# Performance work log

Measured on AMD Instinct MI355X. Metric: run time of the kernel, lower is better.

Reference implementation:

```python
import jax, jax.numpy as jnp
import numpy as np

# Conv2d config matching init_kwargs
STRIDE = (1, 1)
PADDING = (1, 1)
DILATION = (1, 1)


def setup_inputs() -> dict:
    key = jax.random.key(0)
    k1, k2, k3 = jax.random.split(key, 3)
    B, Cin, H, W_ = 32, 128, 56, 56
    Cout, KH, KW = 256, 3, 3
    x = jax.random.normal(k1, (B, Cin, H, W_), dtype=jnp.float32)
    # original init: uniform(-stdv, stdv), stdv = 1/sqrt(Cin*KH*KW)
    stdv = 1.0 / np.sqrt(Cin * KH * KW)
    W = jax.random.uniform(k2, (Cout, Cin, KH, KW), dtype=jnp.float32, minval=-stdv, maxval=stdv)
    b = jax.random.uniform(k3, (Cout,), dtype=jnp.float32, minval=-stdv, maxval=stdv)
    return {"x": x, "W": W, "b": b}


def reference(x, W, b):
    # Same math as unfold(im2col) + GEMM + bias: a standard 2D convolution.
    out = jax.lax.conv_general_dilated(
        x, W,
        window_strides=STRIDE,
        padding=[(PADDING[0], PADDING[0]), (PADDING[1], PADDING[1])],
        rhs_dilation=DILATION,
        dimension_numbers=("NCHW", "OIHW", "NCHW"),
    )
    return out + b[None, :, None, None]
```

## Files before the change

kernel.cpp:

```cpp
#include <hip/hip_runtime.h>

typedef unsigned short ushort_t;
typedef __attribute__((ext_vector_type(8))) short bf16x8;
typedef __attribute__((ext_vector_type(4))) float f32x4;
typedef __attribute__((ext_vector_type(4))) unsigned short ushort4v;

constexpr int BATCH = 32, CIN = 128, H = 56, W = 56, COUT = 256;
constexpr int HP = 58, WP = 58;
constexpr int KTOT = CIN * 9;
constexpr size_t WB_BYTES = (size_t)COUT * KTOT * 2;
constexpr int PLANE = BATCH * HP * WP;
constexpr size_t XP_BYTES = (size_t)16 * PLANE * 8 * 2;

__device__ inline ushort_t f2bf(float f) {
  union { float fl; unsigned u; } v; v.fl = f;
  unsigned u = v.u;
  return (ushort_t)((u + 0x7fffu + ((u >> 16) & 1u)) >> 16);
}


__global__ void conv_w(const float* __restrict__ Ws, ushort_t* __restrict__ Wb2) {
  int idx = blockIdx.x * 256 + threadIdx.x;
  int c = idx & 7;
  int cout = (idx >> 3) & 255;
  int kb = (idx >> 11) & 7;
  int t = idx >> 14;
  int pos = t >> 1, half = t & 1;
  int cin = half * 64 + kb * 8 + c;
  Wb2[idx] = f2bf(Ws[(cout * 128 + cin) * 9 + pos]);
}

__global__ void xpad2(const float* __restrict__ x, ushort_t* __restrict__ xp2) {
  __shared__ ushort_t tile[128][58];
  int bh = blockIdx.x;
  int b = bh / 58, h = bh - b * 58;
  bool interior = (h >= 1 && h <= 56);
  if (interior) {
    int hIn = h - 1;
    const float4* x4 = (const float4*)x;
    {
      int ch = threadIdx.x & 127, side = threadIdx.x >> 7;
      tile[ch][side * 57] = 0;
    }
    for (int it = 0; it < 7; ++it) {
      int i = it * 256 + (int)threadIdx.x;
      int ch = i / 14, q = i - ch * 14;
      float4 v = x4[(size_t)(b * 128 + ch) * 784 + hIn * 14 + q];
      int wb = 1 + q * 4;
      tile[ch][wb + 0] = f2bf(v.x);
      tile[ch][wb + 1] = f2bf(v.y);
      tile[ch][wb + 2] = f2bf(v.z);
      tile[ch][wb + 3] = f2bf(v.w);
    }
  }
  __syncthreads();
  ushort4v* o4 = (ushort4v*)xp2;
  for (int it = 0; it < 8; ++it) {
    int i = it * 256 + (int)threadIdx.x;
    if (i >= 1856) break;
    int c8 = i / 116, r = i - c8 * 116;
    int w = r >> 1, hf = r & 1;
    ushort4v v;
    if (interior) {
      int ch = c8 * 8 + hf * 4;
      v.x = tile[ch + 0][w];
      v.y = tile[ch + 1][w];
      v.z = tile[ch + 2][w];
      v.w = tile[ch + 3][w];
    } else {
      v.x = v.y = v.z = v.w = 0;
    }
    o4[((size_t)((c8 * 32 + b) * 58 + h) * 58 + w) * 2 + hf] = v;
  }
}


__global__ __launch_bounds__(256, 2) void conv_mfma(
    const ushort_t* __restrict__ Wb2, const ushort_t* __restrict__ xp2,
    const float* __restrict__ bias, float* __restrict__ out) {
  __shared__ ushort_t ldsA[2][8192];
  __shared__ ushort_t ldsB[2][8192];

  const int tid = threadIdx.x;
  const int lane = tid & 63;
  const int wid = tid >> 6;
  const int wm = wid >> 1, wn = wid & 1;
  const int lg = lane >> 4, lr = lane & 15;
  const int tileN = blockIdx.x;
  const int blkM = blockIdx.y;

  const int srow = tid & 127;
  const int hi = tid >> 7;

  const ushort_t* aPre[4];
  const ushort_t* bPre[4];
  {
    int pg = tileN * 128 + srow;
    int bq = pg / 3136;
    int rem = pg - bq * 3136;
    int hh = rem / 56;
    int wwp = rem - hh * 56;
    int pixBase = (bq * 58 + hh) * 58 + wwp;
#pragma unroll
    for (int p = 0; p < 4; ++p) {
      int kb = p * 2 + hi;
      aPre[p] = Wb2 + kb * 2048 + blkM * 1024 + srow * 8;
      bPre[p] = xp2 + ((size_t)kb * PLANE + pixBase) * 8;
    }
  }
  const int dOff = tid * 8;

  f32x4 acc[4][4] = {};

  auto stage = [&](int bb, int t) {
    int pos = t >> 1;
    int kh = pos / 3;
    int kw = pos - kh * 3;
    int aoff = t * 16384;
    int xoff = ((t & 1) * (8 * PLANE) + kh * 58 + kw) * 8;
    ushort_t* dA = &ldsA[bb][0];
    ushort_t* dB = &ldsB[bb][0];
#pragma unroll
    for (int p = 0; p < 4; ++p) {
      __builtin_amdgcn_global_load_lds(
          (const __attribute__((address_space(1))) unsigned int*)(aPre[p] + aoff),
          (__attribute__((address_space(3))) unsigned int*)(dA + p * 2048 + dOff),
          16, 0, 0);
      __builtin_amdgcn_global_load_lds(
          (const __attribute__((address_space(1))) unsigned int*)(bPre[p] + xoff),
          (__attribute__((address_space(3))) unsigned int*)(dB + p * 2048 + dOff),
          16, 0, 0);
    }
  };

  auto compute = [&](int bb) {
    const ushort_t* A0 = &ldsA[bb][0];
    const ushort_t* B0 = &ldsB[bb][0];
#pragma unroll
    for (int ks = 0; ks < 2; ++ks) {
      const int kb = ks * 4 + lg;
      bf16x8 av[4], bv[4];
#pragma unroll
      for (int m = 0; m < 4; ++m)
        av[m] = *(const bf16x8*)(A0 + kb * 1024 + (wm * 64 + m * 16 + lr) * 8);
#pragma unroll
      for (int n = 0; n < 4; ++n)
        bv[n] = *(const bf16x8*)(B0 + kb * 1024 + (wn * 64 + n * 16 + lr) * 8);
#pragma unroll
      for (int m = 0; m < 4; ++m)
#pragma unroll
        for (int n = 0; n < 4; ++n)
          acc[m][n] = __builtin_amdgcn_mfma_f32_16x16x32_bf16(av[m], bv[n], acc[m][n], 0, 0, 0);
    }
  };

  stage(0, 0);
  int bb = 0;
  for (int t = 0; t < 18; ++t) {
    __syncthreads();
    if (t < 17) stage(bb ^ 1, t + 1);
    compute(bb);
    bb ^= 1;
  }

  const int cb = blkM * 128 + wm * 64 + lg * 4;
  float bvv[4][4];
#pragma unroll
  for (int m = 0; m < 4; ++m)
#pragma unroll
    for (int r = 0; r < 4; ++r) bvv[m][r] = bias[cb + m * 16 + r];

#pragma unroll
  for (int n = 0; n < 4; ++n) {
    int pgo = tileN * 128 + wn * 64 + n * 16 + lr;
    int bq2 = pgo / 3136;
    int rem2 = pgo - bq2 * 3136;
    float* op = out + (size_t)bq2 * 256 * 3136 + rem2;
#pragma unroll
    for (int m = 0; m < 4; ++m)
#pragma unroll
      for (int r = 0; r < 4; ++r)
        op[(size_t)(cb + m * 16 + r) * 3136] = acc[m][n][r] + bvv[m][r];
  }
}

__global__ void conv_naive(const float* __restrict__ x, const float* __restrict__ Wt,
                           const float* __restrict__ bias, float* __restrict__ out, int total) {
  int idx = blockIdx.x * 256 + threadIdx.x;
  if (idx >= total) return;
  int w = idx % 56;
  int t1 = idx / 56;
  int h = t1 % 56;
  int t2 = t1 / 56;
  int co = t2 % 256;
  int b = t2 / 256;
  float acc = bias[co];
  for (int c = 0; c < 128; ++c)
    for (int kh = 0; kh < 3; ++kh) {
      int ih = h + kh - 1;
      if (ih < 0 || ih >= 56) continue;
      for (int kw = 0; kw < 3; ++kw) {
        int iw = w + kw - 1;
        if (iw < 0 || iw >= 56) continue;
        acc += x[((b * 128 + c) * 56 + ih) * 56 + iw] * Wt[((co * 128 + c) * 3 + kh) * 3 + kw];
      }
    }
  out[idx] = acc;
}

extern "C" void kernel_launch(void* const* d_in, const int* in_sizes, int n_in,
                              void* d_out, int out_size, void* d_ws, size_t ws_size,
                              hipStream_t stream) {
  const float* x = (const float*)d_in[0];
  const float* Wt = (const float*)d_in[1];
  const float* bias = (const float*)d_in[2];
  float* out = (float*)d_out;

  const size_t need = WB_BYTES + XP_BYTES;
  if (ws_size < need) {
    int total = BATCH * COUT * H * W;
    conv_naive<<<(total + 255) / 256, 256, 0, stream>>>(x, Wt, bias, out, total);
    return;
  }
  ushort_t* Wb2 = (ushort_t*)d_ws;
  ushort_t* xp2 = (ushort_t*)((char*)d_ws + WB_BYTES);

  conv_w<<<1152, 256, 0, stream>>>(Wt, Wb2);
  xpad2<<<32 * 58, 256, 0, stream>>>(x, xp2);
  dim3 grid(784, 2);
  conv_mfma<<<grid, 256, 0, stream>>>(Wb2, xp2, bias, out);
}
```

Baseline: 230.7 us.

## Enlarge conv GEMM tile to 256x256 with 512 threads and prefetch two stages ahead

The implicit-GEMM conv kernel now uses 512-thread blocks, each covering all 256 output channels and 256 pixels. This replaces the 128x128 tiles spread over a 784x2 grid. Each wave computes an 8x4 grid of MFMA tiles, which raises compute per LDS read and means each pixel tile is loaded once instead of twice. The loop is restructured so global-to-LDS loads for step t+2 are issued after a barrier, overlapping with the second k-half of MFMAs, with explicit vmcnt waits and raised wave priority during the MFMA burst. The risks are 128 accumulator registers per thread, lower occupancy with 128KB of LDS per block, and only 392 blocks to fill the GPU.

```diff
diff --git a/kernel.cpp b/kernel.cpp
--- a/kernel.cpp
+++ b/kernel.cpp
@@ -75,109 +75,133 @@
 }
 
 
-__global__ __launch_bounds__(256, 2) void conv_mfma(
+__global__ __launch_bounds__(512) void conv_mfma(
     const ushort_t* __restrict__ Wb2, const ushort_t* __restrict__ xp2,
     const float* __restrict__ bias, float* __restrict__ out) {
-  __shared__ ushort_t ldsA[2][8192];
-  __shared__ ushort_t ldsB[2][8192];
+  __shared__ ushort_t ldsA[2][16384];
+  __shared__ ushort_t ldsB[2][16384];
 
   const int tid = threadIdx.x;
   const int lane = tid & 63;
   const int wid = tid >> 6;
-  const int wm = wid >> 1, wn = wid & 1;
+  const int wm = wid >> 2, wn = wid & 3;
   const int lg = lane >> 4, lr = lane & 15;
   const int tileN = blockIdx.x;
-  const int blkM = blockIdx.y;
-
-  const int srow = tid & 127;
-  const int hi = tid >> 7;
-
-  const ushort_t* aPre[4];
-  const ushort_t* bPre[4];
-  {
-    int pg = tileN * 128 + srow;
+
+  const ushort_t* aSrc[4];
+  const ushort_t* bSrc[4];
+#pragma unroll
+  for (int p = 0; p < 4; ++p) {
+    int idx = p * 512 + tid;
+    aSrc[p] = Wb2 + idx * 8;
+    int kb = idx >> 8, pi = idx & 255;
+    int pg = tileN * 256 + pi;
     int bq = pg / 3136;
     int rem = pg - bq * 3136;
     int hh = rem / 56;
-    int wwp = rem - hh * 56;
-    int pixBase = (bq * 58 + hh) * 58 + wwp;
-#pragma unroll
-    for (int p = 0; p < 4; ++p) {
-      int kb = p * 2 + hi;
-      aPre[p] = Wb2 + kb * 2048 + blkM * 1024 + srow * 8;
-      bPre[p] = xp2 + ((size_t)kb * PLANE + pixBase) * 8;
-    }
+    int ww = rem - hh * 56;
+    int pixBase = (bq * 58 + hh) * 58 + ww;
+    bSrc[p] = xp2 + ((size_t)kb * PLANE + pixBase) * 8;
   }
   const int dOff = tid * 8;
-
-  f32x4 acc[4][4] = {};
 
   auto stage = [&](int bb, int t) {
     int pos = t >> 1;
     int kh = pos / 3;
     int kw = pos - kh * 3;
     int aoff = t * 16384;
-    int xoff = ((t & 1) * (8 * PLANE) + kh * 58 + kw) * 8;
+    int boff = (t & 1) * (8 * PLANE * 8) + (kh * 58 + kw) * 8;
     ushort_t* dA = &ldsA[bb][0];
     ushort_t* dB = &ldsB[bb][0];
 #pragma unroll
     for (int p = 0; p < 4; ++p) {
       __builtin_amdgcn_global_load_lds(
-          (const __attribute__((address_space(1))) unsigned int*)(aPre[p] + aoff),
-          (__attribute__((address_space(3))) unsigned int*)(dA + p * 2048 + dOff),
+          (const __attribute__((address_space(1))) unsigned int*)(aSrc[p] + aoff),
+          (__attribute__((address_space(3))) unsigned int*)(dA + p * 4096 + dOff),
           16, 0, 0);
       __builtin_amdgcn_global_load_lds(
-          (const __attribute__((address_space(1))) unsigned int*)(bPre[p] + xoff),
-          (__attribute__((address_space(3))) unsigned int*)(dB + p * 2048 + dOff),
+          (const __attribute__((address_space(1))) unsigned int*)(bSrc[p] + boff),
+          (__attribute__((address_space(3))) unsigned int*)(dB + p * 4096 + dOff),
           16, 0, 0);
     }
   };
 
-  auto compute = [&](int bb) {
-    const ushort_t* A0 = &ldsA[bb][0];
-    const ushort_t* B0 = &ldsB[bb][0];
-#pragma unroll
-    for (int ks = 0; ks < 2; ++ks) {
-      const int kb = ks * 4 + lg;
-      bf16x8 av[4], bv[4];
-#pragma unroll
-      for (int m = 0; m < 4; ++m)
-        av[m] = *(const bf16x8*)(A0 + kb * 1024 + (wm * 64 + m * 16 + lr) * 8);
-#pragma unroll
-      for (int n = 0; n < 4; ++n)
-        bv[n] = *(const bf16x8*)(B0 + kb * 1024 + (wn * 64 + n * 16 + lr) * 8);
-#pragma unroll
-      for (int m = 0; m < 4; ++m)
-#pragma unroll
-        for (int n = 0; n < 4; ++n)
-          acc[m][n] = __builtin_amdgcn_mfma_f32_16x16x32_bf16(av[m], bv[n], acc[m][n], 0, 0, 0);
-    }
-  };
+  f32x4 acc[8][4] = {};
 
   stage(0, 0);
-  int bb = 0;
+  stage(1, 1);
+  asm volatile("s_waitcnt vmcnt(8)" ::: "memory");
+  __builtin_amdgcn_s_barrier();
+
   for (int t = 0; t < 18; ++t) {
-    __syncthreads();
-    if (t < 17) stage(bb ^ 1, t + 1);
-    compute(bb);
-    bb ^= 1;
-  }
-
-  const int cb = blkM * 128 + wm * 64 + lg * 4;
-  float bvv[4][4];
-#pragma unroll
-  for (int m = 0; m < 4; ++m)
+    const int p = t & 1;
+    const ushort_t* A0 = &ldsA[p][0];
+    const ushort_t* B0 = &ldsB[p][0];
+
+    bf16x8 a0[8], b0[4];
+    {
+      const int kb = lg;
+#pragma unroll
+      for (int m = 0; m < 8; ++m)
+        a0[m] = *(const bf16x8*)(A0 + kb * 2048 + (wm * 128 + m * 16 + lr) * 8);
+#pragma unroll
+      for (int n = 0; n < 4; ++n)
+        b0[n] = *(const bf16x8*)(B0 + kb * 2048 + (wn * 64 + n * 16 + lr) * 8);
+    }
+#pragma unroll
+    for (int m = 0; m < 8; ++m)
+#pragma unroll
+      for (int n = 0; n < 4; ++n)
+        acc[m][n] = __builtin_amdgcn_mfma_f32_16x16x32_bf16(a0[m], b0[n], acc[m][n], 0, 0, 0);
+
+    bf16x8 a1[8], b1[4];
+    {
+      const int kb = 4 + lg;
+#pragma unroll
+      for (int m = 0; m < 8; ++m)
+        a1[m] = *(const bf16x8*)(A0 + kb * 2048 + (wm * 128 + m * 16 + lr) * 8);
+#pragma unroll
+      for (int n = 0; n < 4; ++n)
+        b1[n] = *(const bf16x8*)(B0 + kb * 2048 + (wn * 64 + n * 16 + lr) * 8);
+    }
+
+    asm volatile("s_waitcnt lgkmcnt(0)" ::: "memory");
+    __builtin_amdgcn_sched_barrier(0);
+    __builtin_amdgcn_s_barrier();
+    __builtin_amdgcn_sched_barrier(0);
+    if (t < 16) stage(p, t + 2);
+
+    __builtin_amdgcn_s_setprio(1);
+#pragma unroll
+    for (int m = 0; m < 8; ++m)
+#pragma unroll
+      for (int n = 0; n < 4; ++n)
+        acc[m][n] = __builtin_amdgcn_mfma_f32_16x16x32_bf16(a1[m], b1[n], acc[m][n], 0, 0, 0);
+    __builtin_amdgcn_s_setprio(0);
+
+    if (t < 16) {
+      asm volatile("s_waitcnt vmcnt(8)" ::: "memory");
+    } else if (t == 16) {
+      asm volatile("s_waitcnt vmcnt(0)" ::: "memory");
+    }
+    __builtin_amdgcn_s_barrier();
+  }
+
+  const int cb = wm * 128 + lg * 4;
+  float bvv[8][4];
+#pragma unroll
+  for (int m = 0; m < 8; ++m)
 #pragma unroll
     for (int r = 0; r < 4; ++r) bvv[m][r] = bias[cb + m * 16 + r];
 
 #pragma unroll
   for (int n = 0; n < 4; ++n) {
-    int pgo = tileN * 128 + wn * 64 + n * 16 + lr;
+    int pgo = tileN * 256 + wn * 64 + n * 16 + lr;
     int bq2 = pgo / 3136;
     int rem2 = pgo - bq2 * 3136;
     float* op = out + (size_t)bq2 * 256 * 3136 + rem2;
 #pragma unroll
-    for (int m = 0; m < 4; ++m)
+    for (int m = 0; m < 8; ++m)
 #pragma unroll
       for (int r = 0; r < 4; ++r)
         op[(size_t)(cb + m * 16 + r) * 3136] = acc[m][n][r] + bvv[m][r];
@@ -227,6 +251,5 @@
 
   conv_w<<<1152, 256, 0, stream>>>(Wt, Wb2);
   xpad2<<<32 * 58, 256, 0, stream>>>(x, xp2);
-  dim3 grid(784, 2);
-  conv_mfma<<<grid, 256, 0, stream>>>(Wb2, xp2, bias, out);
-}
+  conv_mfma<<<392, 512, 0, stream>>>(Wb2, xp2, bias, out);
+}
```

New measurement: 213.3 us. 1.08x faster.
